# Performance work log

Hardware: AMD Instinct MI355X
Metric: run time of the kernel (lower is better)

Reference implementation:

```python
import jax, jax.numpy as jnp
import numpy as np

D_MODEL = 1024
NUM_HEADS = 16
HEAD_DIM = D_MODEL // NUM_HEADS  # 64
M_BITS = 32
B, N = 4, 2048


def setup_inputs() -> dict:
    key = jax.random.key(0)
    ks = jax.random.split(key, 6)
    s = 1.0 / np.sqrt(D_MODEL)
    se = 1.0 / np.sqrt(HEAD_DIM)
    return {
        "x": jax.random.normal(ks[0], (B, N, D_MODEL), dtype=jnp.float32),
        "Wq": jax.random.normal(ks[1], (D_MODEL, D_MODEL), dtype=jnp.float32) * s,
        "Wk": jax.random.normal(ks[2], (D_MODEL, D_MODEL), dtype=jnp.float32) * s,
        "Wv": jax.random.normal(ks[3], (D_MODEL, D_MODEL), dtype=jnp.float32) * s,
        # per-head witness (bit) encoders: project head_dim -> m_bits
        "W_enc": jax.random.normal(ks[4], (NUM_HEADS, HEAD_DIM, M_BITS), dtype=jnp.float32) * se,
        "Wo": jax.random.normal(ks[5], (D_MODEL, D_MODEL), dtype=jnp.float32) * s,
    }


def reference(x, Wq, Wk, Wv, W_enc, Wo):
    Bsz, Nq, _ = x.shape
    # QKV projections (nn.Linear, no bias): y = x @ W^T
    Q = x @ Wq.T
    K = x @ Wk.T  # self-attention: context = x
    V = x @ Wv.T
    # split heads: [B, N, H, hd]
    Qh = Q.reshape(Bsz, Nq, NUM_HEADS, HEAD_DIM)
    Kh = K.reshape(Bsz, Nq, NUM_HEADS, HEAD_DIM)
    Vh = V.reshape(Bsz, Nq, NUM_HEADS, HEAD_DIM)
    # witness encodings: soft-bit (tanh of random-hyperplane projections), m_bits << head_dim feature space
    q_enc = jnp.tanh(jnp.einsum("bnhd,hdm->bnhm", Qh, W_enc))
    k_enc = jnp.tanh(jnp.einsum("bnhd,hdm->bnhm", Kh, W_enc))
    # witness similarity scores over m_bits instead of full head_dim
    scale = 1.0 / np.sqrt(M_BITS)
    scores = jnp.einsum("bnhm,bkhm->bhnk", q_enc, k_enc) * scale  # [B,H,N,N]
    attn = jax.nn.softmax(scores, axis=-1)
    out = jnp.einsum("bhnk,bkhd->bnhd", attn, Vh).reshape(Bsz, Nq, D_MODEL)
    return out @ Wo.T
```

## Files before the change

kernel.cpp:

```cpp
#include <hip/hip_runtime.h>

typedef unsigned short u16;
typedef unsigned int u32;

typedef __bf16 bfrag __attribute__((ext_vector_type(8)));
typedef float f32x4 __attribute__((ext_vector_type(4)));
typedef float f32x16 __attribute__((ext_vector_type(16)));
typedef float f32x2 __attribute__((ext_vector_type(2)));

__device__ __forceinline__ float b2f(u16 h) {
    u32 u = ((u32)h) << 16;
    return __builtin_bit_cast(float, u);
}
__device__ __forceinline__ u16 f2b(float f) {
    u32 u = __builtin_bit_cast(u32, f);
    u += 0x7fffu + ((u >> 16) & 1u);
    return (u16)(u >> 16);
}
__device__ __forceinline__ u32 cvtpk(float lo, float hi) {
    u32 r;
    asm("v_cvt_pk_bf16_f32 %0, %1, %2" : "=v"(r) : "v"(lo), "v"(hi));
    return r;
}

#if defined(__has_builtin)
#if __has_builtin(__builtin_amdgcn_exp2f)
#define EXP2(x) __builtin_amdgcn_exp2f(x)
#endif
#endif
#ifndef EXP2
#define EXP2(x) exp2f(x)
#endif

#if defined(__has_builtin)
#if __has_builtin(__builtin_amdgcn_global_load_lds)
#define HAS_GLL 1
#endif
#endif
#ifndef HAS_GLL
#define HAS_GLL 0
#endif

#if HAS_GLL
typedef __attribute__((address_space(1))) const u32 as1_u32;
typedef __attribute__((address_space(3))) u32 as3_u32;
__device__ __forceinline__ void gl_lds16(const u16* g, u16* l) {
    __builtin_amdgcn_global_load_lds((as1_u32*)g, (as3_u32*)l, 16, 0, 0);
}
#endif

#if defined(__has_builtin)
#if __has_builtin(__builtin_amdgcn_permlane32_swap)
#define HAS_PLS 1
#endif
#endif
#ifndef HAS_PLS
#define HAS_PLS 0
#endif

__device__ __forceinline__ void plswap(u32 a, u32 b, u32& o0, u32& o1) {
#if HAS_PLS
    auto r = __builtin_amdgcn_permlane32_swap((int)a, (int)b, false, false);
    o0 = (u32)r[0];
    o1 = (u32)r[1];
#else
    int idx = ((int)(threadIdx.x & 63) ^ 32) << 2;
    u32 ca = (u32)__builtin_amdgcn_ds_bpermute(idx, (int)a);
    u32 cb = (u32)__builtin_amdgcn_ds_bpermute(idx, (int)b);
    bool hi = (threadIdx.x & 63) >= 32;
    o0 = hi ? cb : a;
    o1 = hi ? b : ca;
#endif
}

#define BATCH 4
#define SEQ   2048
#define DM    1024
#define NH    16
#define HD    64
#define MB    32
#define STOK  (BATCH * SEQ)

#define QSCALE 0.25503524337503433f
#define TWOLOG2E 2.8853900817779268f

__device__ __forceinline__ void storeC(u16* C, size_t idx, float v)   { C[idx] = f2b(v); }
__device__ __forceinline__ void storeC(float* C, size_t idx, float v) { C[idx] = v; }

__global__ __launch_bounds__(256) void cvt_f32_bf16(
    const float* __restrict__ s, u16* __restrict__ d, int n8)
{
    int i = blockIdx.x * 256 + threadIdx.x;
    if (i >= n8) return;
    const float4* sp = (const float4*)s + (size_t)i * 2;
    float4 a = sp[0], b = sp[1];
    u16 t[8] = { f2b(a.x), f2b(a.y), f2b(a.z), f2b(a.w),
                 f2b(b.x), f2b(b.y), f2b(b.z), f2b(b.w) };
    ((uint4*)d)[i] = *(uint4*)t;
}

__global__ __launch_bounds__(256) void cvt2_f32_bf16(
    const float* __restrict__ a, const float* __restrict__ b,
    u16* __restrict__ da, u16* __restrict__ db, int n8)
{
    const float* s = blockIdx.y ? b : a;
    u16* d = blockIdx.y ? db : da;
    int i = blockIdx.x * 256 + threadIdx.x;
    if (i >= n8) return;
    const float4* sp = (const float4*)s + (size_t)i * 2;
    float4 x = sp[0], y = sp[1];
    u16 t[8] = { f2b(x.x), f2b(x.y), f2b(x.z), f2b(x.w),
                 f2b(y.x), f2b(y.y), f2b(y.z), f2b(y.w) };
    ((uint4*)d)[i] = *(uint4*)t;
}

__global__ __launch_bounds__(256) void build_cqk(
    const float* __restrict__ Wq, const float* __restrict__ Wk,
    const float* __restrict__ Wenc, u16* __restrict__ CqkT)
{
    const int dblk = blockIdx.x;
    const int qk   = blockIdx.y >> 4;
    const int h    = blockIdx.y & 15;
    const float* W = qk ? Wk : Wq;
    __shared__ float we[64][32];
    const int tid = threadIdx.x;

    for (int p = 0; p < 8; ++p) {
        int idx = p * 256 + tid;
        we[idx >> 5][idx & 31] = Wenc[(size_t)h * (HD * MB) + idx];
    }
    __syncthreads();

    const int mh = tid >> 7;
    const int d  = dblk * 128 + (tid & 127);
    float acc[16] = {};
    for (int dh = 0; dh < 64; ++dh) {
        float w = W[(size_t)(h * 64 + dh) * DM + d];
        for (int m = 0; m < 16; ++m)
            acc[m] += w * we[dh][mh * 16 + m];
    }
    u16* dst = CqkT + (size_t)(qk * 512 + h * 32 + mh * 16) * DM + d;
    for (int m = 0; m < 16; ++m)
        dst[(size_t)m * DM] = f2b(acc[m]);
}

template <int TBM, typename TC>
__global__ __launch_bounds__(256) void gemm_bt(
    const u16* __restrict__ A, const u16* __restrict__ Bt, TC* __restrict__ C,
    int M, int Nc, int K)
{
    constexpr int FI = TBM / 32;
    __shared__ alignas(16) u16 As[TBM * 32];
    __shared__ alignas(16) u16 Bs[128 * 32];

    const int tid  = threadIdx.x;
    const int wave = tid >> 6;
    const int lane = tid & 63;
    const int quad = lane >> 4;
    const int lrow = lane & 15;
    const int bm = blockIdx.y * TBM;
    const int bn = blockIdx.x * 128;
    const int wm = (wave & 1) * (TBM / 2);
    const int wn = (wave >> 1) * 64;

    f32x4 acc[FI][4] = {};

    for (int k0 = 0; k0 < K; k0 += 32) {
#if HAS_GLL
        for (int p = 0; p < TBM / 64; ++p) {
            int cbase = wave * TBM + p * 64;
            int cme   = cbase + lane;
            int row = cme >> 2, col = (cme & 3) * 8;
            gl_lds16(&A[(size_t)(bm + row) * K + k0 + col], &As[(size_t)cbase * 8]);
        }
        for (int p = 0; p < 2; ++p) {
            int cbase = wave * 128 + p * 64;
            int cme   = cbase + lane;
            int row = cme >> 2, col = (cme & 3) * 8;
            gl_lds16(&Bt[(size_t)(bn + row) * K + k0 + col], &Bs[(size_t)cbase * 8]);
        }
#else
        for (int p = 0; p < TBM / 64; ++p) {
            int idx = p * 256 + tid, row = idx >> 2, col = (idx & 3) * 8;
            *(uint4*)&As[row * 32 + col] = *(const uint4*)&A[(size_t)(bm + row) * K + k0 + col];
        }
        for (int p = 0; p < 2; ++p) {
            int idx = p * 256 + tid, row = idx >> 2, col = (idx & 3) * 8;
            *(uint4*)&Bs[row * 32 + col] = *(const uint4*)&Bt[(size_t)(bn + row) * K + k0 + col];
        }
#endif
        __syncthreads();

        bfrag af[FI], bfv[4];
        for (int i = 0; i < FI; ++i)
            af[i] = *(const bfrag*)&As[(wm + i * 16 + lrow) * 32 + quad * 8];
        for (int j = 0; j < 4; ++j)
            bfv[j] = *(const bfrag*)&Bs[(wn + j * 16 + lrow) * 32 + quad * 8];

        for (int i = 0; i < FI; ++i)
            for (int j = 0; j < 4; ++j)
                acc[i][j] = __builtin_amdgcn_mfma_f32_16x16x32_bf16(af[i], bfv[j], acc[i][j], 0, 0, 0);
        __syncthreads();
    }

    for (int i = 0; i < FI; ++i)
        for (int j = 0; j < 4; ++j)
            for (int r = 0; r < 4; ++r) {
                int row = bm + wm + i * 16 + quad * 4 + r;
                int col = bn + wn + j * 16 + lrow;
                storeC(C, (size_t)row * Nc + col, acc[i][j][r]);
            }
}

__global__ __launch_bounds__(256) void gemm_encv(
    const u16* __restrict__ A, const u16* __restrict__ Bt,
    u16* __restrict__ qe, u16* __restrict__ ke, u16* __restrict__ Vt)
{
    __shared__ alignas(16) u16 As[128 * 32];
    __shared__ alignas(16) u16 Bs[128 * 32];

    const int tid  = threadIdx.x;
    const int wave = tid >> 6;
    const int lane = tid & 63;
    const int quad = lane >> 4;
    const int lrow = lane & 15;
    const int bm = blockIdx.y * 128;
    const int bn = blockIdx.x * 128;
    const int wm = (wave & 1) * 64;
    const int wn = (wave >> 1) * 64;

    f32x4 acc[4][4] = {};

    for (int k0 = 0; k0 < DM; k0 += 32) {
#if HAS_GLL
        for (int p = 0; p < 2; ++p) {
            int cbase = wave * 128 + p * 64;
            int cme   = cbase + lane;
            int row = cme >> 2, col = (cme & 3) * 8;
            gl_lds16(&A[(size_t)(bm + row) * DM + k0 + col], &As[(size_t)cbase * 8]);
            gl_lds16(&Bt[(size_t)(bn + row) * DM + k0 + col], &Bs[(size_t)cbase * 8]);
        }
#else
        for (int p = 0; p < 2; ++p) {
            int idx = p * 256 + tid, row = idx >> 2, col = (idx & 3) * 8;
            *(uint4*)&As[row * 32 + col] = *(const uint4*)&A[(size_t)(bm + row) * DM + k0 + col];
            *(uint4*)&Bs[row * 32 + col] = *(const uint4*)&Bt[(size_t)(bn + row) * DM + k0 + col];
        }
#endif
        __syncthreads();

        bfrag af[4], bfv[4];
        for (int i = 0; i < 4; ++i)
            af[i] = *(const bfrag*)&As[(wm + i * 16 + lrow) * 32 + quad * 8];
        for (int j = 0; j < 4; ++j)
            bfv[j] = *(const bfrag*)&Bs[(wn + j * 16 + lrow) * 32 + quad * 8];

        for (int i = 0; i < 4; ++i)
            for (int j = 0; j < 4; ++j)
                acc[i][j] = __builtin_amdgcn_mfma_f32_16x16x32_bf16(af[i], bfv[j], acc[i][j], 0, 0, 0);
        __syncthreads();
    }

    if (bn < 1024) {
        for (int i = 0; i < 4; ++i)
            for (int j = 0; j < 4; ++j) {
                int col = bn + wn + j * 16 + lrow;
                int hh = (col >> 5) & 15;
                int mm = col & 31;
                u16* dst = (col < 512) ? qe : ke;
                float qs = (col < 512) ? QSCALE : 1.0f;
                for (int r = 0; r < 4; ++r) {
                    int row = bm + wm + i * 16 + quad * 4 + r;
                    int bb = row >> 11, nn = row & 2047;
                    float e = EXP2(acc[i][j][r] * TWOLOG2E);
                    float t = (1.f - 2.f / (e + 1.f)) * qs;
                    dst[((size_t)(bb * NH + hh) * SEQ + nn) * MB + mm] = f2b(t);
                }
            }
    } else {
        for (int i = 0; i < 4; ++i)
            for (int j = 0; j < 4; ++j) {
                int col = bn - 1024 + wn + j * 16 + lrow;
                int hh = col >> 6, dd = col & 63;
                int row0 = bm + wm + i * 16 + quad * 4;
                int bb = row0 >> 11, nn = row0 & 2047;
                u16 t4[4] = { f2b(acc[i][j][0]), f2b(acc[i][j][1]),
                              f2b(acc[i][j][2]), f2b(acc[i][j][3]) };
                *(uint2*)&Vt[((size_t)(bb * NH + hh) * HD + dd) * SEQ + nn] = *(uint2*)t4;
            }
    }
}

__global__ __launch_bounds__(256, 4) void flash_attn(
    const u16* __restrict__ qe,
    const u16* __restrict__ ke,
    const u16* __restrict__ Vt,
    u16* __restrict__ AO)
{
    const int h = blockIdx.x, b = blockIdx.y, qt = blockIdx.z;
    const int tid  = threadIdx.x;
    const int wave = tid >> 6;
    const int lane = tid & 63;
    const int r31  = lane & 31;
    const int hi   = lane >> 5;

    __shared__ alignas(16) u16 Kt[2][64 * 32];
    __shared__ alignas(16) u16 Vtile[2][64 * 64];

    const size_t bhh = (size_t)(b * NH + h);
    const u16* keb = ke + bhh * SEQ * MB;
    const u16* qeb = qe + bhh * SEQ * MB;
    const u16* vtb = Vt + bhh * HD * SEQ;

    const int q0w = qt * 128 + wave * 32;

    const int klr = tid >> 2;
    const int ksl = tid & 3;
    const u16* ksrc = keb + (size_t)klr * MB + ((ksl ^ (klr & 3)) * 8);
    const int d0 = wave * 8 + (lane >> 3);
    const int c0 = lane & 7;
    const int g0 = (c0 ^ (d0 & 7)) * 8;
    const u16* vsrc0 = vtb + (size_t)d0 * SEQ + g0;
    const u16* vsrc1 = vtb + (size_t)(d0 + 32) * SEQ + g0;

#if HAS_GLL
    gl_lds16(ksrc,  Kt[0] + wave * 512);
    gl_lds16(vsrc0, Vtile[0] + wave * 512);
    gl_lds16(vsrc1, Vtile[0] + 2048 + wave * 512);
#else
    *(uint4*)&Kt[0][klr * 32 + ksl * 8] = *(const uint4*)ksrc;
    *(uint4*)&Vtile[0][d0 * 64 + c0 * 8] = *(const uint4*)vsrc0;
    *(uint4*)&Vtile[0][(d0 + 32) * 64 + c0 * 8] = *(const uint4*)vsrc1;
#endif
    ksrc += 64 * MB;
    vsrc0 += 64;
    vsrc1 += 64;

    bfrag qf[2];
    {
        const u16* qrow = qeb + (size_t)(q0w + r31) * MB;
        qf[0] = *(const bfrag*)&qrow[hi * 8];
        qf[1] = *(const bfrag*)&qrow[16 + hi * 8];
    }

    const f32x16 zero16 = {};

    f32x16 Oa[2] = {};
    f32x2 dacc = {0.f, 0.f};
    const int ksw = r31 & 3;
    const int vsw = r31 & 7;

    for (int c = 0; c < 32; ++c) {
        const int cur = c & 1, nxt = cur ^ 1;
        __syncthreads();

        if (c + 1 < 32) {
#if HAS_GLL
            gl_lds16(ksrc,  Kt[nxt] + wave * 512);
            gl_lds16(vsrc0, Vtile[nxt] + wave * 512);
            gl_lds16(vsrc1, Vtile[nxt] + 2048 + wave * 512);
#else
            *(uint4*)&Kt[nxt][klr * 32 + ksl * 8] = *(const uint4*)ksrc;
            *(uint4*)&Vtile[nxt][d0 * 64 + c0 * 8] = *(const uint4*)vsrc0;
            *(uint4*)&Vtile[nxt][(d0 + 32) * 64 + c0 * 8] = *(const uint4*)vsrc1;
#endif
            ksrc += 64 * MB;
            vsrc0 += 64;
            vsrc1 += 64;
        }

        const u16* KtC = Kt[cur];
        const u16* VtC = Vtile[cur];

        bfrag kf[2][2];
        for (int kt = 0; kt < 2; ++kt) {
            const u16* krow = &KtC[(kt * 32 + r31) * 32];
            kf[kt][0] = *(const bfrag*)&krow[((hi    ) ^ ksw) * 8];
            kf[kt][1] = *(const bfrag*)&krow[((2 + hi) ^ ksw) * 8];
        }

        bfrag pf[2][2];
        for (int kt = 0; kt < 2; ++kt) {
            __builtin_amdgcn_s_setprio(1);
            f32x16 St = __builtin_amdgcn_mfma_f32_32x32x16_bf16(kf[kt][0], qf[0], zero16, 0, 0, 0);
            St = __builtin_amdgcn_mfma_f32_32x32x16_bf16(kf[kt][1], qf[1], St, 0, 0, 0);
            __builtin_amdgcn_s_setprio(0);
            for (int kc = 0; kc < 2; ++kc) {
                float e0 = EXP2(St[8 * kc + 0]);
                float e1 = EXP2(St[8 * kc + 1]);
                float e2 = EXP2(St[8 * kc + 2]);
                float e3 = EXP2(St[8 * kc + 3]);
                float e4 = EXP2(St[8 * kc + 4]);
                float e5 = EXP2(St[8 * kc + 5]);
                float e6 = EXP2(St[8 * kc + 6]);
                float e7 = EXP2(St[8 * kc + 7]);
                f32x2 p0 = {e0, e1}, p1 = {e2, e3}, p2 = {e4, e5}, p3 = {e6, e7};
                dacc += (p0 + p1) + (p2 + p3);
                u32 A0 = cvtpk(e0, e1), A1 = cvtpk(e2, e3);
                u32 B0 = cvtpk(e4, e5), B1 = cvtpk(e6, e7);
                u32 w0, w1, w2, w3;
                plswap(A0, B0, w0, w2);
                plswap(A1, B1, w1, w3);
                uint4 words = { w0, w1, w2, w3 };
                pf[kt][kc] = __builtin_bit_cast(bfrag, words);
            }
        }

        __builtin_amdgcn_s_setprio(1);
        for (int dt = 0; dt < 2; ++dt) {
            const u16* vrow = &VtC[(dt * 32 + r31) * 64];
            for (int kt = 0; kt < 2; ++kt)
                for (int kc = 0; kc < 2; ++kc) {
                    bfrag vf = *(const bfrag*)&vrow[(((kt * 4 + kc * 2 + hi) ^ vsw) * 8)];
                    Oa[dt] = __builtin_amdgcn_mfma_f32_32x32x16_bf16(vf, pf[kt][kc], Oa[dt], 0, 0, 0);
                }
        }
        __builtin_amdgcn_s_setprio(0);
    }

    float dsum = dacc[0] + dacc[1];
    u32 o0, o1;
    plswap(__builtin_bit_cast(u32, dsum), __builtin_bit_cast(u32, dsum), o0, o1);
    float den = __builtin_bit_cast(float, o0) + __builtin_bit_cast(float, o1);

    {
        float inv = 1.0f / den;
        u16* aob = AO + (size_t)(b * SEQ + q0w + r31) * DM + h * HD;
        for (int dt = 0; dt < 2; ++dt)
            for (int g = 0; g < 4; ++g) {
                u16 t4[4] = { f2b(Oa[dt][g * 4 + 0] * inv),
                              f2b(Oa[dt][g * 4 + 1] * inv),
                              f2b(Oa[dt][g * 4 + 2] * inv),
                              f2b(Oa[dt][g * 4 + 3] * inv) };
                *(uint2*)&aob[dt * 32 + g * 8 + hi * 4] = *(uint2*)t4;
            }
    }
}

extern "C" void kernel_launch(void* const* d_in, const int* in_sizes, int n_in,
                              void* d_out, int out_size, void* d_ws, size_t ws_size,
                              hipStream_t stream) {
    const float* x    = (const float*)d_in[0];
    const float* Wq   = (const float*)d_in[1];
    const float* Wk   = (const float*)d_in[2];
    const float* Wv   = (const float*)d_in[3];
    const float* Wenc = (const float*)d_in[4];
    const float* Wo   = (const float*)d_in[5];
    float* out = (float*)d_out;

    const size_t MB1 = (size_t)1024 * 1024;
    char* ws = (char*)d_ws;
    u16* AO   = (u16*)(ws);
    u16* Wo_b = (u16*)(ws + 16 * MB1);
    u16* Bc   = (u16*)(ws + 18 * MB1);
    u16* Vt   = (u16*)(ws + 24 * MB1);
    u16* qe   = (u16*)(ws + 48 * MB1);
    u16* ke   = (u16*)(ws + 56 * MB1);

    u16* xb = (u16*)d_out;
    u16* wvb = Bc + (size_t)1024 * DM;

    cvt_f32_bf16<<<dim3(STOK * DM / 8 / 256), 256, 0, stream>>>(x, xb, STOK * DM / 8);
    cvt2_f32_bf16<<<dim3(DM * DM / 8 / 256, 2), 256, 0, stream>>>(Wv, Wo, wvb, Wo_b, DM * DM / 8);
    build_cqk<<<dim3(8, 32), 256, 0, stream>>>(Wq, Wk, Wenc, Bc);

    gemm_encv<<<dim3(2048 / 128, STOK / 128), 256, 0, stream>>>(xb, Bc, qe, ke, Vt);

    flash_attn<<<dim3(NH, BATCH, SEQ / 128), 256, 0, stream>>>(qe, ke, Vt, AO);

    gemm_bt<64, float><<<dim3(DM / 128, STOK / 64), 256, 0, stream>>>(AO, Wo_b, out, STOK, DM, DM);
}
```

Baseline: 259.5 us.

## Rewrite flash attention as single-wave blocks loading K/V fragments directly into registers

The attention kernel drops shared-memory double buffering and block-wide barriers. Each 64-thread block now handles 32 queries and loads K and V MFMA fragments straight from global memory into registers, using a two-stage register prefetch. This removes the LDS traffic and __syncthreads overhead, but K/V tiles are no longer shared across four waves, so the global/L2 read volume per query rises and the direct loads may be less coalesced.

```diff
diff --git a/kernel.cpp b/kernel.cpp
--- a/kernel.cpp
+++ b/kernel.cpp
@@ -291,131 +291,104 @@
     }
 }
 
-__global__ __launch_bounds__(256, 4) void flash_attn(
+__device__ __forceinline__ void fa_ld(const u16* kb, const u16* vb, int k0,
+    bfrag& kf0, bfrag& kf1, bfrag& v00, bfrag& v01, bfrag& v10, bfrag& v11)
+{
+    const u16* kr = kb + (size_t)k0 * MB;
+    kf0 = *(const bfrag*)(kr);
+    kf1 = *(const bfrag*)(kr + 16);
+    const u16* vr = vb + k0;
+    v00 = *(const bfrag*)(vr);
+    v01 = *(const bfrag*)(vr + 16);
+    v10 = *(const bfrag*)(vr + 32 * SEQ);
+    v11 = *(const bfrag*)(vr + 32 * SEQ + 16);
+}
+
+__device__ __forceinline__ void fa_step(
+    bfrag kf0, bfrag kf1, bfrag v00, bfrag v01, bfrag v10, bfrag v11,
+    bfrag qf0, bfrag qf1, f32x16& Oa0, f32x16& Oa1, f32x2& dacc)
+{
+    const f32x16 zero16 = {};
+    __builtin_amdgcn_s_setprio(1);
+    f32x16 St = __builtin_amdgcn_mfma_f32_32x32x16_bf16(kf0, qf0, zero16, 0, 0, 0);
+    St = __builtin_amdgcn_mfma_f32_32x32x16_bf16(kf1, qf1, St, 0, 0, 0);
+    __builtin_amdgcn_s_setprio(0);
+    bfrag pf0, pf1;
+    {
+        float e0 = EXP2(St[0]), e1 = EXP2(St[1]), e2 = EXP2(St[2]), e3 = EXP2(St[3]);
+        float e4 = EXP2(St[4]), e5 = EXP2(St[5]), e6 = EXP2(St[6]), e7 = EXP2(St[7]);
+        f32x2 p0 = {e0, e1}, p1 = {e2, e3}, p2 = {e4, e5}, p3 = {e6, e7};
+        dacc += (p0 + p1) + (p2 + p3);
+        u32 A0 = cvtpk(e0, e1), A1 = cvtpk(e2, e3);
+        u32 B0 = cvtpk(e4, e5), B1 = cvtpk(e6, e7);
+        u32 w0, w1, w2, w3;
+        plswap(A0, B0, w0, w2);
+        plswap(A1, B1, w1, w3);
+        uint4 words = { w0, w1, w2, w3 };
+        pf0 = __builtin_bit_cast(bfrag, words);
+    }
+    {
+        float e0 = EXP2(St[8]),  e1 = EXP2(St[9]),  e2 = EXP2(St[10]), e3 = EXP2(St[11]);
+        float e4 = EXP2(St[12]), e5 = EXP2(St[13]), e6 = EXP2(St[14]), e7 = EXP2(St[15]);
+        f32x2 p0 = {e0, e1}, p1 = {e2, e3}, p2 = {e4, e5}, p3 = {e6, e7};
+        dacc += (p0 + p1) + (p2 + p3);
+        u32 A0 = cvtpk(e0, e1), A1 = cvtpk(e2, e3);
+        u32 B0 = cvtpk(e4, e5), B1 = cvtpk(e6, e7);
+        u32 w0, w1, w2, w3;
+        plswap(A0, B0, w0, w2);
+        plswap(A1, B1, w1, w3);
+        uint4 words = { w0, w1, w2, w3 };
+        pf1 = __builtin_bit_cast(bfrag, words);
+    }
+    __builtin_amdgcn_s_setprio(1);
+    Oa0 = __builtin_amdgcn_mfma_f32_32x32x16_bf16(v00, pf0, Oa0, 0, 0, 0);
+    Oa0 = __builtin_amdgcn_mfma_f32_32x32x16_bf16(v01, pf1, Oa0, 0, 0, 0);
+    Oa1 = __builtin_amdgcn_mfma_f32_32x32x16_bf16(v10, pf0, Oa1, 0, 0, 0);
+    Oa1 = __builtin_amdgcn_mfma_f32_32x32x16_bf16(v11, pf1, Oa1, 0, 0, 0);
+    __builtin_amdgcn_s_setprio(0);
+}
+
+__global__ __launch_bounds__(64, 3) void flash_attn(
     const u16* __restrict__ qe,
     const u16* __restrict__ ke,
     const u16* __restrict__ Vt,
     u16* __restrict__ AO)
 {
     const int h = blockIdx.x, b = blockIdx.y, qt = blockIdx.z;
-    const int tid  = threadIdx.x;
-    const int wave = tid >> 6;
-    const int lane = tid & 63;
+    const int lane = threadIdx.x & 63;
     const int r31  = lane & 31;
     const int hi   = lane >> 5;
-
-    __shared__ alignas(16) u16 Kt[2][64 * 32];
-    __shared__ alignas(16) u16 Vtile[2][64 * 64];
 
     const size_t bhh = (size_t)(b * NH + h);
     const u16* keb = ke + bhh * SEQ * MB;
     const u16* qeb = qe + bhh * SEQ * MB;
     const u16* vtb = Vt + bhh * HD * SEQ;
 
-    const int q0w = qt * 128 + wave * 32;
-
-    const int klr = tid >> 2;
-    const int ksl = tid & 3;
-    const u16* ksrc = keb + (size_t)klr * MB + ((ksl ^ (klr & 3)) * 8);
-    const int d0 = wave * 8 + (lane >> 3);
-    const int c0 = lane & 7;
-    const int g0 = (c0 ^ (d0 & 7)) * 8;
-    const u16* vsrc0 = vtb + (size_t)d0 * SEQ + g0;
-    const u16* vsrc1 = vtb + (size_t)(d0 + 32) * SEQ + g0;
-
-#if HAS_GLL
-    gl_lds16(ksrc,  Kt[0] + wave * 512);
-    gl_lds16(vsrc0, Vtile[0] + wave * 512);
-    gl_lds16(vsrc1, Vtile[0] + 2048 + wave * 512);
-#else
-    *(uint4*)&Kt[0][klr * 32 + ksl * 8] = *(const uint4*)ksrc;
-    *(uint4*)&Vtile[0][d0 * 64 + c0 * 8] = *(const uint4*)vsrc0;
-    *(uint4*)&Vtile[0][(d0 + 32) * 64 + c0 * 8] = *(const uint4*)vsrc1;
-#endif
-    ksrc += 64 * MB;
-    vsrc0 += 64;
-    vsrc1 += 64;
-
-    bfrag qf[2];
+    const int q0 = qt * 32;
+
+    bfrag qf0, qf1;
     {
-        const u16* qrow = qeb + (size_t)(q0w + r31) * MB;
-        qf[0] = *(const bfrag*)&qrow[hi * 8];
-        qf[1] = *(const bfrag*)&qrow[16 + hi * 8];
-    }
-
-    const f32x16 zero16 = {};
-
-    f32x16 Oa[2] = {};
+        const u16* qrow = qeb + (size_t)(q0 + r31) * MB + hi * 8;
+        qf0 = *(const bfrag*)(qrow);
+        qf1 = *(const bfrag*)(qrow + 16);
+    }
+
+    const u16* kb_ = keb + (size_t)r31 * MB + hi * 8;
+    const u16* vb_ = vtb + (size_t)r31 * SEQ + hi * 8;
+
+    f32x16 Oa0 = {}, Oa1 = {};
     f32x2 dacc = {0.f, 0.f};
-    const int ksw = r31 & 3;
-    const int vsw = r31 & 7;
-
-    for (int c = 0; c < 32; ++c) {
-        const int cur = c & 1, nxt = cur ^ 1;
-        __syncthreads();
-
-        if (c + 1 < 32) {
-#if HAS_GLL
-            gl_lds16(ksrc,  Kt[nxt] + wave * 512);
-            gl_lds16(vsrc0, Vtile[nxt] + wave * 512);
-            gl_lds16(vsrc1, Vtile[nxt] + 2048 + wave * 512);
-#else
-            *(uint4*)&Kt[nxt][klr * 32 + ksl * 8] = *(const uint4*)ksrc;
-            *(uint4*)&Vtile[nxt][d0 * 64 + c0 * 8] = *(const uint4*)vsrc0;
-            *(uint4*)&Vtile[nxt][(d0 + 32) * 64 + c0 * 8] = *(const uint4*)vsrc1;
-#endif
-            ksrc += 64 * MB;
-            vsrc0 += 64;
-            vsrc1 += 64;
-        }
-
-        const u16* KtC = Kt[cur];
-        const u16* VtC = Vtile[cur];
-
-        bfrag kf[2][2];
-        for (int kt = 0; kt < 2; ++kt) {
-            const u16* krow = &KtC[(kt * 32 + r31) * 32];
-            kf[kt][0] = *(const bfrag*)&krow[((hi    ) ^ ksw) * 8];
-            kf[kt][1] = *(const bfrag*)&krow[((2 + hi) ^ ksw) * 8];
-        }
-
-        bfrag pf[2][2];
-        for (int kt = 0; kt < 2; ++kt) {
-            __builtin_amdgcn_s_setprio(1);
-            f32x16 St = __builtin_amdgcn_mfma_f32_32x32x16_bf16(kf[kt][0], qf[0], zero16, 0, 0, 0);
-            St = __builtin_amdgcn_mfma_f32_32x32x16_bf16(kf[kt][1], qf[1], St, 0, 0, 0);
-            __builtin_amdgcn_s_setprio(0);
-            for (int kc = 0; kc < 2; ++kc) {
-                float e0 = EXP2(St[8 * kc + 0]);
-                float e1 = EXP2(St[8 * kc + 1]);
-                float e2 = EXP2(St[8 * kc + 2]);
-                float e3 = EXP2(St[8 * kc + 3]);
-                float e4 = EXP2(St[8 * kc + 4]);
-                float e5 = EXP2(St[8 * kc + 5]);
-                float e6 = EXP2(St[8 * kc + 6]);
-                float e7 = EXP2(St[8 * kc + 7]);
-                f32x2 p0 = {e0, e1}, p1 = {e2, e3}, p2 = {e4, e5}, p3 = {e6, e7};
-                dacc += (p0 + p1) + (p2 + p3);
-                u32 A0 = cvtpk(e0, e1), A1 = cvtpk(e2, e3);
-                u32 B0 = cvtpk(e4, e5), B1 = cvtpk(e6, e7);
-                u32 w0, w1, w2, w3;
-                plswap(A0, B0, w0, w2);
-                plswap(A1, B1, w1, w3);
-                uint4 words = { w0, w1, w2, w3 };
-                pf[kt][kc] = __builtin_bit_cast(bfrag, words);
-            }
-        }
-
-        __builtin_amdgcn_s_setprio(1);
-        for (int dt = 0; dt < 2; ++dt) {
-            const u16* vrow = &VtC[(dt * 32 + r31) * 64];
-            for (int kt = 0; kt < 2; ++kt)
-                for (int kc = 0; kc < 2; ++kc) {
-                    bfrag vf = *(const bfrag*)&vrow[(((kt * 4 + kc * 2 + hi) ^ vsw) * 8)];
-                    Oa[dt] = __builtin_amdgcn_mfma_f32_32x32x16_bf16(vf, pf[kt][kc], Oa[dt], 0, 0, 0);
-                }
-        }
-        __builtin_amdgcn_s_setprio(0);
+
+    bfrag ka0, ka1, va00, va01, va10, va11;
+    bfrag kb0, kb1, vb00, vb01, vb10, vb11;
+
+    fa_ld(kb_, vb_, 0, ka0, ka1, va00, va01, va10, va11);
+    for (int c = 0; c < 64; c += 2) {
+        fa_ld(kb_, vb_, (c + 1) * 32, kb0, kb1, vb00, vb01, vb10, vb11);
+        fa_step(ka0, ka1, va00, va01, va10, va11, qf0, qf1, Oa0, Oa1, dacc);
+        if (c + 2 < 64)
+            fa_ld(kb_, vb_, (c + 2) * 32, ka0, ka1, va00, va01, va10, va11);
+        fa_step(kb0, kb1, vb00, vb01, vb10, vb11, qf0, qf1, Oa0, Oa1, dacc);
     }
 
     float dsum = dacc[0] + dacc[1];
@@ -425,13 +398,14 @@
 
     {
         float inv = 1.0f / den;
-        u16* aob = AO + (size_t)(b * SEQ + q0w + r31) * DM + h * HD;
+        u16* aob = AO + (size_t)(b * SEQ + q0 + r31) * DM + h * HD;
+        const f32x16* Oas[2] = { &Oa0, &Oa1 };
         for (int dt = 0; dt < 2; ++dt)
             for (int g = 0; g < 4; ++g) {
-                u16 t4[4] = { f2b(Oa[dt][g * 4 + 0] * inv),
-                              f2b(Oa[dt][g * 4 + 1] * inv),
-                              f2b(Oa[dt][g * 4 + 2] * inv),
-                              f2b(Oa[dt][g * 4 + 3] * inv) };
+                u16 t4[4] = { f2b((*Oas[dt])[g * 4 + 0] * inv),
+                              f2b((*Oas[dt])[g * 4 + 1] * inv),
+                              f2b((*Oas[dt])[g * 4 + 2] * inv),
+                              f2b((*Oas[dt])[g * 4 + 3] * inv) };
                 *(uint2*)&aob[dt * 32 + g * 8 + hi * 4] = *(uint2*)t4;
             }
     }
@@ -466,7 +440,7 @@
 
     gemm_encv<<<dim3(2048 / 128, STOK / 128), 256, 0, stream>>>(xb, Bc, qe, ke, Vt);
 
-    flash_attn<<<dim3(NH, BATCH, SEQ / 128), 256, 0, stream>>>(qe, ke, Vt, AO);
+    flash_attn<<<dim3(NH, BATCH, SEQ / 32), 64, 0, stream>>>(qe, ke, Vt, AO);
 
     gemm_bt<64, float><<<dim3(DM / 128, STOK / 64), 256, 0, stream>>>(AO, Wo_b, out, STOK, DM, DM);
 }
```

Measured after the change: 342.8 us. 32.1% more time.
